# Kernel tuning notes

Measured on AMD Instinct MI355X. Metric: run time of the kernel, lower is better.

The kernel has to match this reference:

```python
import jax, jax.numpy as jnp
import numpy as np

TOP_K = 2

def setup_inputs() -> dict:
    key = jax.random.key(0)
    ks = jax.random.split(key, 8)
    B, S, D = 2, 2048, 1024
    N_r, N_s = 16, 2
    u = jax.random.normal(ks[0], (B, S, D), dtype=jnp.float32)
    centroids = jax.random.normal(ks[1], (N_r, D), dtype=jnp.float32)
    expert_biases = jnp.zeros((N_r,), dtype=jnp.float32)
    # routed expert Linear params: y = u @ W.T + b, W stored [E, d_out, d_in]
    Wr = jax.random.normal(ks[2], (N_r, D, D), dtype=jnp.float32) * (1.0 / np.sqrt(D))
    br = jax.random.normal(ks[3], (N_r, D), dtype=jnp.float32) * 0.01
    Ws = jax.random.normal(ks[4], (N_s, D, D), dtype=jnp.float32) * (1.0 / np.sqrt(D))
    bs = jax.random.normal(ks[5], (N_s, D), dtype=jnp.float32) * 0.01
    return {"u": u, "centroids": centroids, "expert_biases": expert_biases,
            "Wr": Wr, "br": br, "Ws": Ws, "bs": bs}

def reference(u, centroids, expert_biases, Wr, br, Ws, bs):
    N_r = centroids.shape[0]
    N_s = Ws.shape[0]
    # routing scores over experts
    raw_scores = jnp.einsum('bsd,ed->bse', u, centroids)          # [B,S,E]
    s = jax.nn.softmax(raw_scores + expert_biases, axis=-1)
    # scatter top-k softmax values (un-renormalized, as in the source) into gates
    topk_vals, topk_idx = jax.lax.top_k(s, TOP_K)                  # [B,S,K]
    g_topk = jnp.sum(jax.nn.one_hot(topk_idx, N_r, dtype=s.dtype) * topk_vals[..., None], axis=-2)  # [B,S,E]
    # dense per-expert Linear for all tokens, then gated combine (faithful to source)
    xe = jnp.einsum('bsd,eod->bseo', u, Wr) + br                   # [B,S,E,D]
    routed = jnp.einsum('bse,bseo->bso', g_topk, xe)               # [B,S,D]
    # shared experts: mean of N_s dense Linears
    shared = (jnp.einsum('bsd,eod->bso', u, Ws) + jnp.sum(bs, axis=0)) / N_s
    return u + routed + shared
```

## Files before the change

kernel.cpp:

```cpp
#include <hip/hip_runtime.h>

typedef unsigned short u16x8 __attribute__((ext_vector_type(8)));
typedef short          s16x8 __attribute__((ext_vector_type(8)));
typedef float          f32x4 __attribute__((ext_vector_type(4)));

#define NTOK   4096
#define DMODEL 1024
#define NEXP   16
#define TOPK   2
#define BK     32
#define NK     (DMODEL / BK)
#define MAXT   128

__device__ inline unsigned short f2bf(float f) {
    unsigned int x = __float_as_uint(f);
    x += 0x7fffu + ((x >> 16) & 1u);
    return (unsigned short)(x >> 16);
}

__device__ inline void gld16(const void* g, void* l) {
    __builtin_amdgcn_global_load_lds(
        (const __attribute__((address_space(1))) void*)g,
        (__attribute__((address_space(3))) void*)l, 16, 0, 0);
}

__global__ void routing_kernel(const float* __restrict__ u,
                               const float* __restrict__ cent,
                               const float* __restrict__ ebias,
                               float* __restrict__ topk_g,
                               int*   __restrict__ topk_i,
                               unsigned short* __restrict__ ub) {
    int wid  = threadIdx.x >> 6;
    int lane = threadIdx.x & 63;
    int t = blockIdx.x * 4 + wid;
    const float* urow = u + (size_t)t * DMODEL;

    double acc[NEXP];
#pragma unroll
    for (int e = 0; e < NEXP; e++) acc[e] = 0.0;

    for (int j = 0; j < DMODEL / 64; j++) {
        int d = j * 64 + lane;
        float uf = urow[d];
        ub[(size_t)t * DMODEL + d] = f2bf(uf);
        double uv = (double)uf;
#pragma unroll
        for (int e = 0; e < NEXP; e++)
            acc[e] += uv * (double)cent[e * DMODEL + d];
    }
#pragma unroll
    for (int e = 0; e < NEXP; e++) {
        for (int off = 32; off; off >>= 1)
            acc[e] += __shfl_xor(acc[e], off);
    }
    if (lane == 0) {
        double mx = -1e300;
#pragma unroll
        for (int e = 0; e < NEXP; e++) {
            acc[e] += (double)ebias[e];
            if (acc[e] > mx) mx = acc[e];
        }
        double ex[NEXP], den = 0.0;
#pragma unroll
        for (int e = 0; e < NEXP; e++) { ex[e] = exp(acc[e] - mx); den += ex[e]; }
        int i1 = -1, i2 = -1;
        double v1 = -1.0, v2 = -1.0;
        for (int e = 0; e < NEXP; e++) {
            double v = ex[e];
            if (v > v1)      { v2 = v1; i2 = i1; v1 = v; i1 = e; }
            else if (v > v2) { v2 = v;  i2 = e; }
        }
        topk_g[t * 2 + 0] = (float)(v1 / den);
        topk_g[t * 2 + 1] = (float)(v2 / den);
        topk_i[t * 2 + 0] = i1;
        topk_i[t * 2 + 1] = i2;
    }
}

__global__ void build_all(const float* __restrict__ topk_g,
                          const int*   __restrict__ topk_i,
                          int* __restrict__ cnt,
                          int* __restrict__ tokL,
                          float* __restrict__ gateL,
                          int* __restrict__ idL,
                          int* __restrict__ desc,
                          int* __restrict__ numT) {
    __shared__ int scnt[NEXP];
    int tid = threadIdx.x;
    if (tid < NEXP) scnt[tid] = 0;
    __syncthreads();
    for (int id = tid; id < NTOK * TOPK; id += 1024) {
        int e = topk_i[id];
        int pos = atomicAdd(&scnt[e], 1);
        tokL[e * NTOK + pos]  = id >> 1;
        gateL[e * NTOK + pos] = topk_g[id];
        idL[e * NTOK + pos]   = id;
    }
    __syncthreads();
    if (tid == 0) {
        int s = 0;
        for (int mt = 0; mt < NTOK / 128; mt++) desc[s++] = (NEXP << 16) | mt;
        for (int e = 0; e < NEXP; e++) {
            cnt[e] = scnt[e];
            int nt = (scnt[e] + 127) >> 7;
            for (int m = 0; m < nt; m++) desc[s++] = (e << 16) | m;
        }
        numT[0] = s;
    }
}

#define NWR8  (NEXP * DMODEL * DMODEL / 8)
#define NWS8  (DMODEL * DMODEL / 8)
#define NB8   ((NEXP + 1) * DMODEL / 8)
__global__ void conv_w(const float* __restrict__ Wr,
                       const float* __restrict__ br,
                       const float* __restrict__ Ws,
                       const float* __restrict__ bs,
                       unsigned short* __restrict__ w17,
                       float* __restrict__ b17) {
    int id = blockIdx.x * 256 + threadIdx.x;
    if (id < NWR8) {
        size_t base = (size_t)id * 8;
        u16x8 o;
#pragma unroll
        for (int i = 0; i < 8; i++) o[i] = f2bf(Wr[base + i]);
        *(u16x8*)&w17[base] = o;
    } else if (id < NWR8 + NWS8) {
        size_t base = (size_t)(id - NWR8) * 8;
        u16x8 o;
#pragma unroll
        for (int i = 0; i < 8; i++)
            o[i] = f2bf(Ws[base + i] + Ws[(size_t)DMODEL * DMODEL + base + i]);
        *(u16x8*)&w17[(size_t)NEXP * DMODEL * DMODEL + base] = o;
    } else if (id < NWR8 + NWS8 + NB8) {
        int base = (id - NWR8 - NWS8) * 8;
#pragma unroll
        for (int i = 0; i < 8; i++) {
            int idx = base + i;
            b17[idx] = idx < NEXP * DMODEL ? br[idx]
                                           : bs[idx - NEXP * DMODEL] + bs[idx - NEXP * DMODEL + DMODEL];
        }
    }
}

__global__ __launch_bounds__(256, 4)
void moe_gemm(const unsigned short* __restrict__ ub,
              const unsigned short* __restrict__ w17,
              const float* __restrict__ b17,
              const int*   __restrict__ cnt,
              const int*   __restrict__ tokL,
              const float* __restrict__ gateL,
              const int*   __restrict__ idL,
              const int*   __restrict__ desc,
              const int*   __restrict__ numT,
              const float* __restrict__ u,
              float* __restrict__ out,
              float* __restrict__ y) {
    int bid = blockIdx.x;
    int tile = bid >> 3;
    int n0 = (bid & 7) * 128;
    if (tile >= numT[0]) return;
    int d = desc[tile];
    int e = d >> 16;
    int row0 = (d & 0xffff) << 7;
    bool is_shared = (e == NEXP);
    int count = is_shared ? NTOK : cnt[e];

    __shared__ __align__(16) unsigned short As[2][128 * BK];
    __shared__ __align__(16) unsigned short Bs[2][128 * BK];

    int t = threadIdx.x;
    int lane = t & 63, wid = t >> 6;
    int wm = wid >> 1, wn = wid & 1;
    int lr = lane & 15, lk4 = lane >> 4;
    int rchunk = (lk4 ^ ((lr >> 1) & 3)) * 8;

    int srow = lane >> 2;
    int scs  = ((lane & 3) ^ ((lane >> 3) & 3)) * 8;

    const int* tl = tokL + e * NTOK;
    const unsigned short* asrc[2];
    const unsigned short* bsrc[2];
    const unsigned short* bb = w17 + (size_t)e * DMODEL * DMODEL + (size_t)n0 * DMODEL;
#pragma unroll
    for (int p = 0; p < 2; p++) {
        int gi = row0 + wid * 32 + p * 16 + srow;
        int tok = is_shared ? gi : tl[gi < count ? gi : count - 1];
        asrc[p] = ub + (size_t)tok * DMODEL + scs;
        bsrc[p] = bb + (size_t)(wid * 32 + p * 16 + srow) * DMODEL + scs;
    }

#define STAGE(buf, kt) do {                                                     \
    int _k0 = (kt) * BK;                                                        \
    _Pragma("unroll")                                                           \
    for (int p = 0; p < 2; p++) {                                               \
        int r = wid * 32 + p * 16;                                              \
        gld16(asrc[p] + _k0, &As[buf][r * BK]);                                 \
        gld16(bsrc[p] + _k0, &Bs[buf][r * BK]);                                 \
    } } while (0)

    f32x4 acc[4][4];
#pragma unroll
    for (int i = 0; i < 4; i++)
#pragma unroll
        for (int j = 0; j < 4; j++)
#pragma unroll
            for (int v = 0; v < 4; v++) acc[i][j][v] = 0.0f;

    STAGE(0, 0);
    int cur = 0;
    for (int kt = 0; kt < NK; kt++) {
        if (kt + 1 < NK) {
            STAGE(cur ^ 1, kt + 1);
            asm volatile("s_waitcnt vmcnt(4)" ::: "memory");
        } else {
            asm volatile("s_waitcnt vmcnt(0)" ::: "memory");
        }
        __builtin_amdgcn_s_barrier();

        __builtin_amdgcn_s_setprio(1);
        s16x8 b[4];
#pragma unroll
        for (int j = 0; j < 4; j++)
            b[j] = *(const s16x8*)&Bs[cur][(wn * 64 + j * 16 + lr) * BK + rchunk];
#pragma unroll
        for (int i = 0; i < 4; i++) {
            s16x8 a = *(const s16x8*)&As[cur][(wm * 64 + i * 16 + lr) * BK + rchunk];
#pragma unroll
            for (int j = 0; j < 4; j++)
                acc[i][j] = __builtin_amdgcn_mfma_f32_16x16x32_bf16(a, b[j], acc[i][j], 0, 0, 0);
        }
        __builtin_amdgcn_s_setprio(0);

        asm volatile("" ::: "memory");
        __builtin_amdgcn_s_barrier();
        cur ^= 1;
    }
#undef STAGE

    const float* be = b17 + e * DMODEL;
    if (is_shared) {
#pragma unroll
        for (int i = 0; i < 4; i++) {
#pragma unroll
            for (int v = 0; v < 4; v++) {
                int row = row0 + wm * 64 + i * 16 + lk4 * 4 + v;
#pragma unroll
                for (int j = 0; j < 4; j++) {
                    int col = n0 + wn * 64 + j * 16 + lr;
                    size_t idx = (size_t)row * DMODEL + col;
                    out[idx] = u[idx] + 0.5f * (acc[i][j][v] + be[col]);
                }
            }
        }
    } else {
#pragma unroll
        for (int i = 0; i < 4; i++) {
#pragma unroll
            for (int v = 0; v < 4; v++) {
                int gi = row0 + wm * 64 + i * 16 + lk4 * 4 + v;
                if (gi < count) {
                    int id = idL[e * NTOK + gi];
                    float g = gateL[e * NTOK + gi];
                    float* yr = y + (size_t)id * DMODEL;
#pragma unroll
                    for (int j = 0; j < 4; j++) {
                        int col = n0 + wn * 64 + j * 16 + lr;
                        yr[col] = g * (acc[i][j][v] + be[col]);
                    }
                }
            }
        }
    }
}

__global__ void combine_kernel(const float* __restrict__ y, float* __restrict__ out) {
    int idx = blockIdx.x * 256 + threadIdx.x;
    size_t base = (size_t)idx * 4;
    int tk = idx >> 8;
    int d4 = idx & 255;
    f32x4 o  = *(const f32x4*)&out[base];
    f32x4 y0 = *(const f32x4*)&y[(size_t)(tk * 2) * DMODEL + d4 * 4];
    f32x4 y1 = *(const f32x4*)&y[(size_t)(tk * 2 + 1) * DMODEL + d4 * 4];
#pragma unroll
    for (int v = 0; v < 4; v++) o[v] += y0[v] + y1[v];
    *(f32x4*)&out[base] = o;
}

extern "C" void kernel_launch(void* const* d_in, const int* in_sizes, int n_in,
                              void* d_out, int out_size, void* d_ws, size_t ws_size,
                              hipStream_t stream) {
    const float* u    = (const float*)d_in[0];
    const float* cent = (const float*)d_in[1];
    const float* eb   = (const float*)d_in[2];
    const float* Wr   = (const float*)d_in[3];
    const float* br   = (const float*)d_in[4];
    const float* Ws   = (const float*)d_in[5];
    const float* bs   = (const float*)d_in[6];
    float* out = (float*)d_out;

    char* ws = (char*)d_ws;
    size_t off = 0;
    auto take = [&](size_t b) { size_t o = off; off += (b + 255) & ~(size_t)255; return o; };
    float* topk_g = (float*)(ws + take(NTOK * TOPK * 4));
    int*   topk_i = (int*)  (ws + take(NTOK * TOPK * 4));
    int*   cnt    = (int*)  (ws + take(64 * 4));
    int*   tokL   = (int*)  (ws + take((size_t)NEXP * NTOK * 4));
    float* gateL  = (float*)(ws + take((size_t)NEXP * NTOK * 4));
    int*   idL    = (int*)  (ws + take((size_t)NEXP * NTOK * 4));
    int*   desc   = (int*)  (ws + take(MAXT * 4));
    int*   numT   = (int*)  (ws + take(64));
    float* b17    = (float*)(ws + take((size_t)(NEXP + 1) * DMODEL * 4));
    unsigned short* ub  = (unsigned short*)(ws + take((size_t)NTOK * DMODEL * 2));
    unsigned short* w17 = (unsigned short*)(ws + take((size_t)(NEXP + 1) * DMODEL * DMODEL * 2));
    float* y = (float*)(ws + take((size_t)NTOK * TOPK * DMODEL * 4));

    routing_kernel<<<NTOK / 4, 256, 0, stream>>>(u, cent, eb, topk_g, topk_i, ub);
    build_all<<<1, 1024, 0, stream>>>(topk_g, topk_i, cnt, tokL, gateL, idL, desc, numT);
    conv_w<<<(NWR8 + NWS8 + NB8 + 255) / 256, 256, 0, stream>>>(Wr, br, Ws, bs, w17, b17);
    moe_gemm<<<8 * MAXT, 256, 0, stream>>>(
        ub, w17, b17, cnt, tokL, gateL, idL, desc, numT, u, out, y);
    combine_kernel<<<(NTOK * DMODEL / 4) / 256, 256, 0, stream>>>(y, out);
}
```

Baseline: 119.5 us.

## Fuse routing and weight conversion, triple-buffer GEMM, store expert outputs in bf16

Merges the routing kernel and the weight conversion kernel into one launch. Routing now appends tokens to the per-expert lists with global atomics, so the single-block build kernel only builds tile descriptors. The GEMM K-loop moves from double to triple buffering with a prefetch distance of two, and its occupancy hint drops to 3 blocks. Per-expert outputs are written as bf16 to halve the intermediate traffic in the combine step, at some cost in precision.

Measured after the change: 195.1 us. 63.3% more time.

```diff
diff --git a/kernel.cpp b/kernel.cpp
--- a/kernel.cpp
+++ b/kernel.cpp
@@ -17,6 +17,10 @@
     x += 0x7fffu + ((x >> 16) & 1u);
     return (unsigned short)(x >> 16);
 }
+__device__ inline float bf2f(unsigned short h) {
+    unsigned int x = ((unsigned int)h) << 16;
+    return __uint_as_float(x);
+}
 
 __device__ inline void gld16(const void* g, void* l) {
     __builtin_amdgcn_global_load_lds(
@@ -24,15 +28,57 @@
         (__attribute__((address_space(3))) void*)l, 16, 0, 0);
 }
 
-__global__ void routing_kernel(const float* __restrict__ u,
-                               const float* __restrict__ cent,
-                               const float* __restrict__ ebias,
-                               float* __restrict__ topk_g,
-                               int*   __restrict__ topk_i,
-                               unsigned short* __restrict__ ub) {
+#define NWR8  (NEXP * DMODEL * DMODEL / 8)
+#define NWS8  (DMODEL * DMODEL / 8)
+#define NB8   ((NEXP + 1) * DMODEL / 8)
+#define RBLK  (NTOK / 4)
+#define CBLK  ((NWR8 + NWS8 + NB8 + 255) / 256)
+
+__global__ void prep_kernel(const float* __restrict__ u,
+                            const float* __restrict__ cent,
+                            const float* __restrict__ ebias,
+                            const float* __restrict__ Wr,
+                            const float* __restrict__ br,
+                            const float* __restrict__ Ws,
+                            const float* __restrict__ bs,
+                            unsigned short* __restrict__ ub,
+                            unsigned short* __restrict__ w17,
+                            float* __restrict__ b17,
+                            int* __restrict__ cnt,
+                            int* __restrict__ tokL,
+                            float* __restrict__ gateL,
+                            int* __restrict__ idL) {
+    int bid = blockIdx.x;
+    if (bid >= RBLK) {
+        int id = (bid - RBLK) * 256 + threadIdx.x;
+        if (id < NWR8) {
+            size_t base = (size_t)id * 8;
+            u16x8 o;
+#pragma unroll
+            for (int i = 0; i < 8; i++) o[i] = f2bf(Wr[base + i]);
+            *(u16x8*)&w17[base] = o;
+        } else if (id < NWR8 + NWS8) {
+            size_t base = (size_t)(id - NWR8) * 8;
+            u16x8 o;
+#pragma unroll
+            for (int i = 0; i < 8; i++)
+                o[i] = f2bf(Ws[base + i] + Ws[(size_t)DMODEL * DMODEL + base + i]);
+            *(u16x8*)&w17[(size_t)NEXP * DMODEL * DMODEL + base] = o;
+        } else if (id < NWR8 + NWS8 + NB8) {
+            int base = (id - NWR8 - NWS8) * 8;
+#pragma unroll
+            for (int i = 0; i < 8; i++) {
+                int idx = base + i;
+                b17[idx] = idx < NEXP * DMODEL
+                    ? br[idx]
+                    : bs[idx - NEXP * DMODEL] + bs[idx - NEXP * DMODEL + DMODEL];
+            }
+        }
+        return;
+    }
     int wid  = threadIdx.x >> 6;
     int lane = threadIdx.x & 63;
-    int t = blockIdx.x * 4 + wid;
+    int t = bid * 4 + wid;
     const float* urow = u + (size_t)t * DMODEL;
 
     double acc[NEXP];
@@ -70,80 +116,32 @@
             if (v > v1)      { v2 = v1; i2 = i1; v1 = v; i1 = e; }
             else if (v > v2) { v2 = v;  i2 = e; }
         }
-        topk_g[t * 2 + 0] = (float)(v1 / den);
-        topk_g[t * 2 + 1] = (float)(v2 / den);
-        topk_i[t * 2 + 0] = i1;
-        topk_i[t * 2 + 1] = i2;
-    }
-}
-
-__global__ void build_all(const float* __restrict__ topk_g,
-                          const int*   __restrict__ topk_i,
-                          int* __restrict__ cnt,
-                          int* __restrict__ tokL,
-                          float* __restrict__ gateL,
-                          int* __restrict__ idL,
-                          int* __restrict__ desc,
-                          int* __restrict__ numT) {
-    __shared__ int scnt[NEXP];
-    int tid = threadIdx.x;
-    if (tid < NEXP) scnt[tid] = 0;
-    __syncthreads();
-    for (int id = tid; id < NTOK * TOPK; id += 1024) {
-        int e = topk_i[id];
-        int pos = atomicAdd(&scnt[e], 1);
-        tokL[e * NTOK + pos]  = id >> 1;
-        gateL[e * NTOK + pos] = topk_g[id];
-        idL[e * NTOK + pos]   = id;
-    }
-    __syncthreads();
-    if (tid == 0) {
+        int p0 = atomicAdd(&cnt[i1], 1);
+        tokL[i1 * NTOK + p0]  = t;
+        gateL[i1 * NTOK + p0] = (float)(v1 / den);
+        idL[i1 * NTOK + p0]   = t * 2;
+        int p1 = atomicAdd(&cnt[i2], 1);
+        tokL[i2 * NTOK + p1]  = t;
+        gateL[i2 * NTOK + p1] = (float)(v2 / den);
+        idL[i2 * NTOK + p1]   = t * 2 + 1;
+    }
+}
+
+__global__ void build_desc(const int* __restrict__ cnt,
+                           int* __restrict__ desc,
+                           int* __restrict__ numT) {
+    if (threadIdx.x == 0) {
         int s = 0;
         for (int mt = 0; mt < NTOK / 128; mt++) desc[s++] = (NEXP << 16) | mt;
         for (int e = 0; e < NEXP; e++) {
-            cnt[e] = scnt[e];
-            int nt = (scnt[e] + 127) >> 7;
+            int nt = (cnt[e] + 127) >> 7;
             for (int m = 0; m < nt; m++) desc[s++] = (e << 16) | m;
         }
         numT[0] = s;
     }
 }
 
-#define NWR8  (NEXP * DMODEL * DMODEL / 8)
-#define NWS8  (DMODEL * DMODEL / 8)
-#define NB8   ((NEXP + 1) * DMODEL / 8)
-__global__ void conv_w(const float* __restrict__ Wr,
-                       const float* __restrict__ br,
-                       const float* __restrict__ Ws,
-                       const float* __restrict__ bs,
-                       unsigned short* __restrict__ w17,
-                       float* __restrict__ b17) {
-    int id = blockIdx.x * 256 + threadIdx.x;
-    if (id < NWR8) {
-        size_t base = (size_t)id * 8;
-        u16x8 o;
-#pragma unroll
-        for (int i = 0; i < 8; i++) o[i] = f2bf(Wr[base + i]);
-        *(u16x8*)&w17[base] = o;
-    } else if (id < NWR8 + NWS8) {
-        size_t base = (size_t)(id - NWR8) * 8;
-        u16x8 o;
-#pragma unroll
-        for (int i = 0; i < 8; i++)
-            o[i] = f2bf(Ws[base + i] + Ws[(size_t)DMODEL * DMODEL + base + i]);
-        *(u16x8*)&w17[(size_t)NEXP * DMODEL * DMODEL + base] = o;
-    } else if (id < NWR8 + NWS8 + NB8) {
-        int base = (id - NWR8 - NWS8) * 8;
-#pragma unroll
-        for (int i = 0; i < 8; i++) {
-            int idx = base + i;
-            b17[idx] = idx < NEXP * DMODEL ? br[idx]
-                                           : bs[idx - NEXP * DMODEL] + bs[idx - NEXP * DMODEL + DMODEL];
-        }
-    }
-}
-
-__global__ __launch_bounds__(256, 4)
+__global__ __launch_bounds__(256, 3)
 void moe_gemm(const unsigned short* __restrict__ ub,
               const unsigned short* __restrict__ w17,
               const float* __restrict__ b17,
@@ -155,7 +153,7 @@
               const int*   __restrict__ numT,
               const float* __restrict__ u,
               float* __restrict__ out,
-              float* __restrict__ y) {
+              unsigned short* __restrict__ y) {
     int bid = blockIdx.x;
     int tile = bid >> 3;
     int n0 = (bid & 7) * 128;
@@ -166,8 +164,8 @@
     bool is_shared = (e == NEXP);
     int count = is_shared ? NTOK : cnt[e];
 
-    __shared__ __align__(16) unsigned short As[2][128 * BK];
-    __shared__ __align__(16) unsigned short Bs[2][128 * BK];
+    __shared__ __align__(16) unsigned short As[3][128 * BK];
+    __shared__ __align__(16) unsigned short Bs[3][128 * BK];
 
     int t = threadIdx.x;
     int lane = t & 63, wid = t >> 6;
@@ -208,33 +206,33 @@
             for (int v = 0; v < 4; v++) acc[i][j][v] = 0.0f;
 
     STAGE(0, 0);
-    int cur = 0;
+    STAGE(1, 1);
+    asm volatile("s_waitcnt vmcnt(4)" ::: "memory");
+    __builtin_amdgcn_s_barrier();
+
+    int cb = 0;
     for (int kt = 0; kt < NK; kt++) {
-        if (kt + 1 < NK) {
-            STAGE(cur ^ 1, kt + 1);
-            asm volatile("s_waitcnt vmcnt(4)" ::: "memory");
-        } else {
-            asm volatile("s_waitcnt vmcnt(0)" ::: "memory");
-        }
-        __builtin_amdgcn_s_barrier();
+        int sb = (cb == 0) ? 2 : cb - 1;
+        if (kt + 2 < NK) STAGE(sb, kt + 2);
 
         __builtin_amdgcn_s_setprio(1);
         s16x8 b[4];
 #pragma unroll
         for (int j = 0; j < 4; j++)
-            b[j] = *(const s16x8*)&Bs[cur][(wn * 64 + j * 16 + lr) * BK + rchunk];
+            b[j] = *(const s16x8*)&Bs[cb][(wn * 64 + j * 16 + lr) * BK + rchunk];
 #pragma unroll
         for (int i = 0; i < 4; i++) {
-            s16x8 a = *(const s16x8*)&As[cur][(wm * 64 + i * 16 + lr) * BK + rchunk];
+            s16x8 a = *(const s16x8*)&As[cb][(wm * 64 + i * 16 + lr) * BK + rchunk];
 #pragma unroll
             for (int j = 0; j < 4; j++)
                 acc[i][j] = __builtin_amdgcn_mfma_f32_16x16x32_bf16(a, b[j], acc[i][j], 0, 0, 0);
         }
         __builtin_amdgcn_s_setprio(0);
 
-        asm volatile("" ::: "memory");
+        if (kt + 2 < NK) asm volatile("s_waitcnt vmcnt(4)" ::: "memory");
+        else             asm volatile("s_waitcnt vmcnt(0)" ::: "memory");
         __builtin_amdgcn_s_barrier();
-        cur ^= 1;
+        cb = (cb == 2) ? 0 : cb + 1;
     }
 #undef STAGE
 
@@ -262,11 +260,11 @@
                 if (gi < count) {
                     int id = idL[e * NTOK + gi];
                     float g = gateL[e * NTOK + gi];
-                    float* yr = y + (size_t)id * DMODEL;
+                    unsigned short* yr = y + (size_t)id * DMODEL;
 #pragma unroll
                     for (int j = 0; j < 4; j++) {
                         int col = n0 + wn * 64 + j * 16 + lr;
-                        yr[col] = g * (acc[i][j][v] + be[col]);
+                        yr[col] = f2bf(g * (acc[i][j][v] + be[col]));
                     }
                 }
             }
@@ -274,17 +272,23 @@
     }
 }
 
-__global__ void combine_kernel(const float* __restrict__ y, float* __restrict__ out) {
+__global__ void combine_kernel(const unsigned short* __restrict__ y,
+                               float* __restrict__ out) {
     int idx = blockIdx.x * 256 + threadIdx.x;
-    size_t base = (size_t)idx * 4;
-    int tk = idx >> 8;
-    int d4 = idx & 255;
-    f32x4 o  = *(const f32x4*)&out[base];
-    f32x4 y0 = *(const f32x4*)&y[(size_t)(tk * 2) * DMODEL + d4 * 4];
-    f32x4 y1 = *(const f32x4*)&y[(size_t)(tk * 2 + 1) * DMODEL + d4 * 4];
-#pragma unroll
-    for (int v = 0; v < 4; v++) o[v] += y0[v] + y1[v];
-    *(f32x4*)&out[base] = o;
+    int tk = idx >> 7;
+    int d8 = (idx & 127) * 8;
+    size_t base = (size_t)tk * DMODEL + d8;
+    u16x8 a = *(const u16x8*)&y[(size_t)(tk * 2) * DMODEL + d8];
+    u16x8 b = *(const u16x8*)&y[(size_t)(tk * 2 + 1) * DMODEL + d8];
+    f32x4 o0 = *(const f32x4*)&out[base];
+    f32x4 o1 = *(const f32x4*)&out[base + 4];
+#pragma unroll
+    for (int v = 0; v < 4; v++) {
+        o0[v] += bf2f(a[v]) + bf2f(b[v]);
+        o1[v] += bf2f(a[v + 4]) + bf2f(b[v + 4]);
+    }
+    *(f32x4*)&out[base] = o0;
+    *(f32x4*)&out[base + 4] = o1;
 }
 
 extern "C" void kernel_launch(void* const* d_in, const int* in_sizes, int n_in,
@@ -302,8 +306,6 @@
     char* ws = (char*)d_ws;
     size_t off = 0;
     auto take = [&](size_t b) { size_t o = off; off += (b + 255) & ~(size_t)255; return o; };
-    float* topk_g = (float*)(ws + take(NTOK * TOPK * 4));
-    int*   topk_i = (int*)  (ws + take(NTOK * TOPK * 4));
     int*   cnt    = (int*)  (ws + take(64 * 4));
     int*   tokL   = (int*)  (ws + take((size_t)NEXP * NTOK * 4));
     float* gateL  = (float*)(ws + take((size_t)NEXP * NTOK * 4));
@@ -313,12 +315,13 @@
     float* b17    = (float*)(ws + take((size_t)(NEXP + 1) * DMODEL * 4));
     unsigned short* ub  = (unsigned short*)(ws + take((size_t)NTOK * DMODEL * 2));
     unsigned short* w17 = (unsigned short*)(ws + take((size_t)(NEXP + 1) * DMODEL * DMODEL * 2));
-    float* y = (float*)(ws + take((size_t)NTOK * TOPK * DMODEL * 4));
-
-    routing_kernel<<<NTOK / 4, 256, 0, stream>>>(u, cent, eb, topk_g, topk_i, ub);
-    build_all<<<1, 1024, 0, stream>>>(topk_g, topk_i, cnt, tokL, gateL, idL, desc, numT);
-    conv_w<<<(NWR8 + NWS8 + NB8 + 255) / 256, 256, 0, stream>>>(Wr, br, Ws, bs, w17, b17);
+    unsigned short* y   = (unsigned short*)(ws + take((size_t)NTOK * TOPK * DMODEL * 2));
+
+    hipMemsetAsync(cnt, 0, 64 * 4, stream);
+    prep_kernel<<<RBLK + CBLK, 256, 0, stream>>>(
+        u, cent, eb, Wr, br, Ws, bs, ub, w17, b17, cnt, tokL, gateL, idL);
+    build_desc<<<1, 64, 0, stream>>>(cnt, desc, numT);
     moe_gemm<<<8 * MAXT, 256, 0, stream>>>(
         ub, w17, b17, cnt, tokL, gateL, idL, desc, numT, u, out, y);
-    combine_kernel<<<(NTOK * DMODEL / 4) / 256, 256, 0, stream>>>(y, out);
-}
+    combine_kernel<<<(NTOK * DMODEL / 8) / 256, 256, 0, stream>>>(y, out);
+}
```
